# Kernel optimization log

Measured on AMD Instinct MI355X. Metric: run time of the kernel, lower is better.

The kernel has to match this reference:

```python
import jax, jax.numpy as jnp
import numpy as np

HID, STEM, BN_OUT, STEM_OUT, MLP = 256, 64, 128, 64, 128
BN_WS, STEM_WS = 5, 17
N, H_BN, W_BN, H_VIS, W_VIS = 4096, 128, 128, 1024, 1024


def setup_inputs() -> dict:
    key = jax.random.key(0)
    ks = jax.random.split(key, 24)
    f32 = jnp.float32
    def rn(k, shape, s=0.05):
        return jax.random.normal(k, shape, f32) * s
    return dict(
        bottleneck=rn(ks[0], (1, HID, H_BN, W_BN), 1.0),
        vis_stem_features=rn(ks[1], (1, STEM, H_VIS, W_VIS), 1.0),
        source_positions_vis=jax.random.uniform(ks[2], (N, 2), f32, 10.0, W_VIS - 10.0),
        pixel_to_sky=rn(ks[3], (N, 2, 2), 0.1),
        fused_h=H_BN, fused_w=W_BN, vis_h=H_VIS, vis_w=W_VIS,
        dw_w=rn(ks[4], (HID, 1, 7, 7)), dw_b=rn(ks[5], (HID,)),
        ln_g=jnp.ones((HID,), f32), ln_b=jnp.zeros((HID,), f32),
        pw1_w=rn(ks[6], (4 * HID, HID)), pw1_b=rn(ks[7], (4 * HID,)),
        pw2_w=rn(ks[8], (HID, 4 * HID)), pw2_b=rn(ks[9], (HID,)),
        cn_gamma=jnp.full((HID,), 1e-2, f32),
        bn1x1_w=rn(ks[10], (BN_OUT, HID, 1, 1)), bn1x1_b=rn(ks[11], (BN_OUT,)),
        st1_w=rn(ks[12], (STEM_OUT, STEM, 3, 3)), st1_b=rn(ks[13], (STEM_OUT,)),
        st2_w=rn(ks[14], (STEM_OUT, STEM_OUT, 3, 3)), st2_b=rn(ks[15], (STEM_OUT,)),
        h1_w=rn(ks[16], (MLP, BN_OUT + STEM_OUT)), h1_b=rn(ks[17], (MLP,)),
        h2_w=rn(ks[18], (MLP, MLP)), h2_b=rn(ks[19], (MLP,)),
        h3_w=rn(ks[20], (3, MLP)),
        h3_b=jnp.array([0.0, 0.0, float(np.log(0.05))], f32),
    )


def _gelu(x):
    return jax.nn.gelu(x, approximate=False)


def _conv2d(x, w, b, padding, groups=1):
    y = jax.lax.conv_general_dilated(
        x, w, (1, 1), [(padding, padding), (padding, padding)],
        dimension_numbers=('NCHW', 'OIHW', 'NCHW'), feature_group_count=groups)
    return y + b[None, :, None, None]


def _bilinear_windows(fm, pos, ws):
    """fm [1,C,H,W], pos [N,2] pixel coords -> [N,C,ws,ws].
    Matches torch grid_sample(mode=bilinear, padding=zeros, align_corners=True)
    with the module's normalize/unnormalize, i.e. direct pixel-coord sampling."""
    C, H, W = fm.shape[1:]
    fm2 = fm[0]
    half = ws // 2
    off = jnp.arange(-half, half + 1, dtype=pos.dtype)
    gy, gx = jnp.meshgrid(off, off, indexing='ij')
    xs = gx[None] + pos[:, 0, None, None]   # [N,ws,ws]
    ys = gy[None] + pos[:, 1, None, None]
    x0 = jnp.floor(xs); y0 = jnp.floor(ys)
    wx1 = xs - x0; wy1 = ys - y0
    x0i = x0.astype(jnp.int32); y0i = y0.astype(jnp.int32)
    def gather(yi, xi, w):
        valid = (yi >= 0) & (yi < H) & (xi >= 0) & (xi < W)
        v = fm2[:, jnp.clip(yi, 0, H - 1), jnp.clip(xi, 0, W - 1)]  # [C,N,ws,ws]
        return v * (w * valid)[None]
    out = (gather(y0i, x0i, (1 - wy1) * (1 - wx1))
           + gather(y0i, x0i + 1, (1 - wy1) * wx1)
           + gather(y0i + 1, x0i, wy1 * (1 - wx1))
           + gather(y0i + 1, x0i + 1, wy1 * wx1))
    return jnp.transpose(out, (1, 0, 2, 3))


def _gauss(ws):
    t = jnp.linspace(-1.0, 1.0, ws)
    yy, xx = jnp.meshgrid(t, t, indexing='ij')
    g = jnp.exp(-(xx ** 2 + yy ** 2) / (2 * 0.4 ** 2))
    return g / g.sum()


def _convnext(x, dw_w, dw_b, ln_g, ln_b, pw1_w, pw1_b, pw2_w, pw2_b, gamma):
    r = x
    x = _conv2d(x, dw_w, dw_b, padding=3, groups=x.shape[1])  # depthwise 7x7
    mu = x.mean(1, keepdims=True)
    var = ((x - mu) ** 2).mean(1, keepdims=True)
    x = (x - mu) / jnp.sqrt(var + 1e-6)
    x = x * ln_g[None, :, None, None] + ln_b[None, :, None, None]
    x = jnp.einsum('nchw,oc->nohw', x, pw1_w) + pw1_b[None, :, None, None]
    x = _gelu(x)
    x = jnp.einsum('nchw,oc->nohw', x, pw2_w) + pw2_b[None, :, None, None]
    return r + gamma[None, :, None, None] * x


def _forward(bottleneck, vis_stem_features, source_positions_vis, pixel_to_sky,
             dw_w, dw_b, ln_g, ln_b, pw1_w, pw1_b, pw2_w, pw2_b, cn_gamma,
             bn1x1_w, bn1x1_b, st1_w, st1_b, st2_w, st2_b,
             h1_w, h1_b, h2_w, h2_b, h3_w, h3_b,
             fused_h, fused_w, vis_h, vis_w):
    scale = jnp.array([fused_w / vis_w, fused_h / vis_h], source_positions_vis.dtype)
    pos_bn = source_positions_vis * scale
    # bottleneck branch: 5x5 windows -> ConvNeXt -> 1x1 conv -> GELU -> gauss pool
    bn_win = _bilinear_windows(bottleneck, pos_bn, BN_WS)              # [N,256,5,5]
    bn_feat = _convnext(bn_win, dw_w, dw_b, ln_g, ln_b, pw1_w, pw1_b, pw2_w, pw2_b, cn_gamma)
    bn_feat = _gelu(_conv2d(bn_feat, bn1x1_w, bn1x1_b, padding=0))     # [N,128,5,5]
    bn_vec = (bn_feat * _gauss(BN_WS)[None, None]).sum((-2, -1))       # [N,128]
    st_win = _bilinear_windows(vis_stem_features, source_positions_vis, STEM_WS)
    st = _gelu(_conv2d(st_win, st1_w, st1_b, padding=1))
    st = _gelu(_conv2d(st, st2_w, st2_b, padding=1))                   # [N,64,17,17]
    st_vec = (st * _gauss(STEM_WS)[None, None]).sum((-2, -1))          # [N,64]
    # head MLP
    x = jnp.concatenate([bn_vec, st_vec], axis=1)                      # [N,192]
    x = _gelu(x @ h1_w.T + h1_b)
    x = _gelu(x @ h2_w.T + h2_b)
    out = x @ h3_w.T + h3_b                                            # [N,3]
    dx_px, dy_px = out[:, 0], out[:, 1]
    log_sigma = jnp.clip(out[:, 2], -6.0, 3.0)
    pix = jnp.stack([dx_px, dy_px], axis=1)                            # [N,2]
    pred_sky = jnp.einsum('nij,nj->ni', pixel_to_sky, pix)             # [N,2]
    confidence = 1.0 / jnp.maximum(jnp.exp(log_sigma), 1e-4)
    return pred_sky, dx_px, dy_px, log_sigma, confidence


def reference(bottleneck, vis_stem_features, source_positions_vis, pixel_to_sky,
              fused_h, fused_w, vis_h, vis_w,
              dw_w, dw_b, ln_g, ln_b, pw1_w, pw1_b, pw2_w, pw2_b, cn_gamma,
              bn1x1_w, bn1x1_b, st1_w, st1_b, st2_w, st2_b,
              h1_w, h1_b, h2_w, h2_b, h3_w, h3_b):
    return _forward(bottleneck, vis_stem_features, source_positions_vis, pixel_to_sky,
                    dw_w, dw_b, ln_g, ln_b, pw1_w, pw1_b, pw2_w, pw2_b, cn_gamma,
                    bn1x1_w, bn1x1_b, st1_w, st1_b, st2_w, st2_b,
                    h1_w, h1_b, h2_w, h2_b, h3_w, h3_b,
                    fused_h, fused_w, vis_h, vis_w)
```

## Files before the change

kernel.cpp:

```cpp
#include <hip/hip_runtime.h>
#include <hip/hip_bf16.h>

#define XSTR 28

typedef short short8 __attribute__((ext_vector_type(8)));
typedef float f32x4  __attribute__((ext_vector_type(4)));
typedef float f32x16 __attribute__((ext_vector_type(16)));

__device__ __forceinline__ float gelu_f(float x){
    return 0.5f*x*(1.0f + erff(x*0.70710678118654752f));
}
__device__ __forceinline__ float gelu_q(float x){
    const float z = 1.5957691216057308f*x*(1.0f + 0.044715f*x*x);
    return x / (1.0f + __expf(-z));
}
__device__ __forceinline__ unsigned short f2bf(float f){
    unsigned int u = __float_as_uint(f);
    u += 0x7fffu + ((u>>16)&1u);
    return (unsigned short)(u>>16);
}
__device__ __forceinline__ unsigned int pack2(float a, float b){
    return (unsigned int)f2bf(a) | ((unsigned int)f2bf(b)<<16);
}
__device__ __forceinline__ float bf_lo(unsigned int u){ return __uint_as_float(u<<16); }
__device__ __forceinline__ float bf_hi(unsigned int u){ return __uint_as_float(u & 0xffff0000u); }
__device__ __forceinline__ float bfu(unsigned short v){ return __uint_as_float(((unsigned int)v)<<16); }

__device__ __forceinline__ void fma_row25(const float* __restrict__ row, float w, float* __restrict__ acc){
    const float4* r4 = (const float4*)row;
    float4 a0=r4[0], a1=r4[1], a2=r4[2], a3=r4[3], a4=r4[4], a5=r4[5];
    float a6 = row[24];
    acc[0]+=a0.x*w;  acc[1]+=a0.y*w;  acc[2]+=a0.z*w;  acc[3]+=a0.w*w;
    acc[4]+=a1.x*w;  acc[5]+=a1.y*w;  acc[6]+=a1.z*w;  acc[7]+=a1.w*w;
    acc[8]+=a2.x*w;  acc[9]+=a2.y*w;  acc[10]+=a2.z*w; acc[11]+=a2.w*w;
    acc[12]+=a3.x*w; acc[13]+=a3.y*w; acc[14]+=a3.z*w; acc[15]+=a3.w*w;
    acc[16]+=a4.x*w; acc[17]+=a4.y*w; acc[18]+=a4.z*w; acc[19]+=a4.w*w;
    acc[20]+=a5.x*w; acc[21]+=a5.y*w; acc[22]+=a5.z*w; acc[23]+=a5.w*w;
    acc[24]+=a6*w;
}

__global__ __launch_bounds__(512,4) void bn_branch_mfma(
    const float* __restrict__ bottleneck, const float* __restrict__ pos,
    const float* __restrict__ dw_w, const float* __restrict__ dw_b,
    const float* __restrict__ ln_g, const float* __restrict__ ln_b,
    const float* __restrict__ pw1_b, const float* __restrict__ pw2_b,
    const float* __restrict__ cn_gamma, const float* __restrict__ bn1x1_b,
    const short8* __restrict__ P1v, const short8* __restrict__ P2v,
    const short8* __restrict__ Pbv,
    float* __restrict__ vec_out)
{
    __shared__ __align__(16) unsigned char Xb[64*512];
    __shared__ __align__(16) unsigned char Hc[64*256];
    __shared__ float redA[400], redB[400], muS[56], rsS[56];

    const int n0 = blockIdx.x*2, t = threadIdx.x;
    const int lane = t & 63, w = t >> 6;
    const int mcol = lane & 15, h4 = lane >> 4;
    const int sP = t >> 8, cP = t & 255;

    unsigned int wvp[13];
    float xdw[25];
    {
        const int n = n0 + sP;
        const float px = pos[2*n]*0.125f, py = pos[2*n+1]*0.125f;
        const float fpx = floorf(px), fpy = floorf(py);
        const int ix0 = (int)fpx - 2, iy0 = (int)fpy - 2;
        const float fx = px - fpx, fy = py - fpy;
        const float w00=(1.f-fy)*(1.f-fx), w01=(1.f-fy)*fx, w10=fy*(1.f-fx), w11=fy*fx;
        float wv[25];
        {
            const float* fm = bottleneck + cP*16384;
            float P[6][6];
            #pragma unroll
            for (int r=0;r<6;r++){
                const int y = iy0+r;
                const bool yok = (y>=0)&&(y<128);
                const int yc = y<0?0:(y>127?127:y);
                #pragma unroll
                for (int s=0;s<6;s++){
                    const int x = ix0+s;
                    const bool ok = yok && (x>=0) && (x<128);
                    const int xc = x<0?0:(x>127?127:x);
                    P[r][s] = ok ? fm[yc*128+xc] : 0.f;
                }
            }
            #pragma unroll
            for (int a=0;a<5;a++)
            #pragma unroll
            for (int b=0;b<5;b++)
                wv[a*5+b] = w00*P[a][b]+w01*P[a][b+1]+w10*P[a+1][b]+w11*P[a+1][b+1];
        }
        #pragma unroll
        for (int i=0;i<12;i++) wvp[i] = pack2(wv[2*i], wv[2*i+1]);
        wvp[12] = pack2(wv[24], 0.f);
        {
            float wcr[49];
            const float* wc = dw_w + cP*49;
            #pragma unroll
            for (int k=0;k<49;k++) wcr[k]=wc[k];
            const float bb = dw_b[cP];
            #pragma unroll
            for (int i=0;i<5;i++){
                #pragma unroll
                for (int j=0;j<5;j++){
                    float a = bb;
                    #pragma unroll
                    for (int u=0;u<7;u++){
                        const int y = i+u-3;
                        if (y<0||y>4) continue;
                        #pragma unroll
                        for (int v=0;v<7;v++){
                            const int x = j+v-3;
                            if (x<0||x>4) continue;
                            a += wv[y*5+x]*wcr[u*7+v];
                        }
                    }
                    xdw[i*5+j] = a;
                }
            }
        }
        #pragma unroll
        for (int p=0;p<25;p++){
            const int row = sP*32 + p;
            *(unsigned short*)(Xb + row*512 + ((2*cP) ^ ((row&7)<<4))) = f2bf(xdw[p]);
        }
    }
    __syncthreads();
    if (t < 400){
        const int sp = t>>3, part = t&7;
        const int row = (sp/25)*32 + (sp - (sp/25)*25);
        float a=0.f, b=0.f;
        for (int c=part; c<256; c+=8){
            const float v = bfu(*(const unsigned short*)(Xb + row*512 + ((2*c) ^ ((row&7)<<4))));
            a += v; b += v*v;
        }
        redA[t]=a; redB[t]=b;
    }
    __syncthreads();
    if (t < 50){
        float a=0.f, b=0.f;
        #pragma unroll
        for (int s=0;s<8;s++){ a+=redA[t*8+s]; b+=redB[t*8+s]; }
        const float m = a*(1.f/256.f);
        const float var = b*(1.f/256.f) - m*m;
        muS[t]=m; rsS[t]=rsqrtf(var+1e-6f);
    }
    __syncthreads();
    {
        const float g = ln_g[cP], bb = ln_b[cP];
        #pragma unroll
        for (int p=0;p<25;p++){
            const int row = sP*32 + p;
            const float v = (xdw[p]-muS[sP*25+p])*rsS[sP*25+p]*g + bb;
            *(unsigned short*)(Xb + row*512 + ((2*cP) ^ ((row&7)<<4))) = f2bf(v);
        }
    }
    __syncthreads();

    f32x4 acc2[2][4];
    #pragma unroll
    for (int ml=0;ml<2;ml++)
        #pragma unroll
        for (int nt=0;nt<4;nt++) acc2[ml][nt]=0.f;

    for (int ch=0; ch<8; ++ch){
        const int mt = ch*8 + w;
        f32x4 a1[4];
        #pragma unroll
        for (int nt=0;nt<4;nt++) a1[nt]=0.f;
        #pragma unroll
        for (int kk=0; kk<8; ++kk){
            const short8 av = P1v[((mt<<3)+kk)*64 + lane];
            #pragma unroll
            for (int nt=0; nt<4; ++nt){
                const int row = nt*16 + mcol;
                const int ad = row*512 + ((kk*64 + h4*16) ^ ((row&7)<<4));
                const short8 bv = *(const short8*)(Xb + ad);
                a1[nt] = __builtin_amdgcn_mfma_f32_16x16x32_bf16(av, bv, a1[nt], 0,0,0);
            }
        }
        {
            const float4 b1v = *(const float4*)(pw1_b + mt*16 + h4*4);
            #pragma unroll
            for (int nt=0; nt<4; ++nt){
                const int row = nt*16 + mcol;
                const float g0 = gelu_q(a1[nt].x + b1v.x);
                const float g1 = gelu_q(a1[nt].y + b1v.y);
                const float g2 = gelu_q(a1[nt].z + b1v.z);
                const float g3 = gelu_q(a1[nt].w + b1v.w);
                const int ad = row*256 + ((w*32 + h4*8) ^ ((row&7)<<4));
                *(uint2*)(Hc + ad) = make_uint2(pack2(g0,g1), pack2(g2,g3));
            }
        }
        __syncthreads();
        #pragma unroll
        for (int ml=0; ml<2; ++ml){
            const int mtc = w*2 + ml;
            #pragma unroll
            for (int kk2=0; kk2<4; ++kk2){
                const short8 av = P2v[(mtc*32 + (ch*4 + kk2))*64 + lane];
                #pragma unroll
                for (int nt=0; nt<4; ++nt){
                    const int row = nt*16 + mcol;
                    const int ad = row*256 + ((kk2*64 + h4*16) ^ ((row&7)<<4));
                    const short8 bv = *(const short8*)(Hc + ad);
                    acc2[ml][nt] = __builtin_amdgcn_mfma_f32_16x16x32_bf16(av, bv, acc2[ml][nt], 0,0,0);
                }
            }
        }
        __syncthreads();
    }

    #pragma unroll
    for (int ml=0; ml<2; ++ml){
        const int c0 = (w*2+ml)*16 + h4*4;
        const float4 gm = *(const float4*)(cn_gamma + c0);
        const float4 b2 = *(const float4*)(pw2_b + c0);
        #pragma unroll
        for (int nt=0; nt<4; ++nt){
            const int row = nt*16 + mcol;
            const int ad = row*512 + ((2*c0) ^ ((row&7)<<4));
            const float f0 = gm.x*(acc2[ml][nt].x + b2.x);
            const float f1 = gm.y*(acc2[ml][nt].y + b2.y);
            const float f2 = gm.z*(acc2[ml][nt].z + b2.z);
            const float f3 = gm.w*(acc2[ml][nt].w + b2.w);
            *(uint2*)(Xb + ad) = make_uint2(pack2(f0,f1), pack2(f2,f3));
        }
    }
    __syncthreads();
    #pragma unroll
    for (int p=0;p<25;p++){
        const int row = sP*32 + p;
        unsigned short* ptr = (unsigned short*)(Xb + row*512 + ((2*cP) ^ ((row&7)<<4)));
        const float r = (p&1) ? bf_hi(wvp[p>>1]) : bf_lo(wvp[p>>1]);
        *ptr = f2bf(bfu(*ptr) + r);
    }
    __syncthreads();

    {
        f32x4 a3[4];
        #pragma unroll
        for (int nt=0;nt<4;nt++) a3[nt]=0.f;
        #pragma unroll
        for (int kk=0; kk<8; ++kk){
            const short8 av = Pbv[((w<<3)+kk)*64 + lane];
            #pragma unroll
            for (int nt=0; nt<4; ++nt){
                const int row = nt*16 + mcol;
                const int ad = row*512 + ((kk*64 + h4*16) ^ ((row&7)<<4));
                const short8 bv = *(const short8*)(Xb + ad);
                a3[nt] = __builtin_amdgcn_mfma_f32_16x16x32_bf16(av, bv, a3[nt], 0,0,0);
            }
        }
        const float4 bb = *(const float4*)(bn1x1_b + w*16 + h4*4);
        float e5[5];
        #pragma unroll
        for (int a=0;a<5;a++){
            const float ta = -1.f + 0.5f*a;
            e5[a] = expf(-3.125f*ta*ta);
        }
        const float Sv = e5[0]+e5[1]+e5[2]+e5[3]+e5[4];
        const float invS = 1.0f/(Sv*Sv);
        float sA[2][4];
        #pragma unroll
        for (int s=0;s<2;s++)
            #pragma unroll
            for (int j=0;j<4;j++) sA[s][j]=0.f;
        #pragma unroll
        for (int nt=0; nt<4; ++nt){
            const int row = nt*16 + mcol;
            const int s = row>>5, p = row&31;
            if (p < 25){
                const int pa = p/5, pb = p - pa*5;
                const float g = e5[pa]*e5[pb];
                sA[s][0] += g*gelu_q(a3[nt].x + bb.x);
                sA[s][1] += g*gelu_q(a3[nt].y + bb.y);
                sA[s][2] += g*gelu_q(a3[nt].z + bb.z);
                sA[s][3] += g*gelu_q(a3[nt].w + bb.w);
            }
        }
        #pragma unroll
        for (int off=1; off<16; off<<=1){
            #pragma unroll
            for (int s=0;s<2;s++)
                #pragma unroll
                for (int j=0;j<4;j++) sA[s][j] += __shfl_xor(sA[s][j], off);
        }
        if (mcol == 0){
            const int o = w*16 + h4*4;
            #pragma unroll
            for (int s=0;s<2;s++){
                float* vo = vec_out + (n0+s)*192 + o;
                vo[0]=sA[s][0]*invS; vo[1]=sA[s][1]*invS;
                vo[2]=sA[s][2]*invS; vo[3]=sA[s][3]*invS;
            }
        }
    }
}

__global__ __launch_bounds__(256) void prepack_bn_kernel(
    const float* __restrict__ W1, const float* __restrict__ W2, const float* __restrict__ Wb,
    unsigned short* __restrict__ P1, unsigned short* __restrict__ P2, unsigned short* __restrict__ Pb)
{
    const int tid = blockIdx.x*256 + threadIdx.x;
    const float* src; unsigned short* dst; int row, col, stride, idx;
    if (tid < 32768){
        idx = tid;
        const int frag = idx>>6, l = idx&63;
        row = (frag>>3)*16 + (l&15); col = (frag&7)*32 + (l>>4)*8; stride = 256;
        src = W1; dst = P1;
    } else if (tid < 65536){
        idx = tid - 32768;
        const int frag = idx>>6, l = idx&63;
        row = (frag>>5)*16 + (l&15); col = (frag&31)*32 + (l>>4)*8; stride = 1024;
        src = W2; dst = P2;
    } else if (tid < 69632){
        idx = tid - 65536;
        const int frag = idx>>6, l = idx&63;
        row = (frag>>3)*16 + (l&15); col = (frag&7)*32 + (l>>4)*8; stride = 256;
        src = Wb; dst = Pb;
    } else return;
    const float* s = src + row*stride + col;
    unsigned int v[4];
    #pragma unroll
    for (int j=0;j<4;j++) v[j] = pack2(s[2*j], s[2*j+1]);
    *(uint4*)(dst + (size_t)idx*8) = make_uint4(v[0],v[1],v[2],v[3]);
}

__global__ __launch_bounds__(256,2) void bn_branch_valu(
    const float* __restrict__ bottleneck, const float* __restrict__ pos,
    const float* __restrict__ dw_w, const float* __restrict__ dw_b,
    const float* __restrict__ ln_g, const float* __restrict__ ln_b,
    const float* __restrict__ pw1_w, const float* __restrict__ pw1_b,
    const float* __restrict__ pw2_w, const float* __restrict__ pw2_b,
    const float* __restrict__ cn_gamma,
    const float* __restrict__ bn1x1_w, const float* __restrict__ bn1x1_b,
    float* __restrict__ vec_out)
{
    __shared__ float xln[256*XSTR];
    __shared__ float hbuf[256*XSTR];
    __shared__ float redA[200], redB[200];
    __shared__ float mu[25], rs[25];

    const int n = blockIdx.x;
    const int t = threadIdx.x;
    const int c = t;

    const float px = pos[2*n]*0.125f, py = pos[2*n+1]*0.125f;
    const float fpx = floorf(px), fpy = floorf(py);
    const int ix0 = (int)fpx - 2, iy0 = (int)fpy - 2;
    const float fx = px - fpx, fy = py - fpy;
    const float w00=(1.f-fy)*(1.f-fx), w01=(1.f-fy)*fx, w10=fy*(1.f-fx), w11=fy*fx;

    float wv[25];
    {
        const float* fm = bottleneck + c*16384;
        float P[6][6];
        #pragma unroll
        for (int r=0;r<6;r++){
            const int y = iy0+r;
            const bool yok = (y>=0)&&(y<128);
            const int yc = y<0?0:(y>127?127:y);
            #pragma unroll
            for (int s=0;s<6;s++){
                const int x = ix0+s;
                const bool ok = yok && (x>=0) && (x<128);
                const int xc = x<0?0:(x>127?127:x);
                P[r][s] = ok ? fm[yc*128+xc] : 0.f;
            }
        }
        #pragma unroll
        for (int a=0;a<5;a++)
        #pragma unroll
        for (int b=0;b<5;b++)
            wv[a*5+b] = w00*P[a][b]+w01*P[a][b+1]+w10*P[a+1][b]+w11*P[a+1][b+1];
    }
    {
        float wcr[49];
        const float* wc = dw_w + c*49;
        #pragma unroll
        for (int k=0;k<49;k++) wcr[k]=wc[k];
        const float bb = dw_b[c];
        #pragma unroll
        for (int i=0;i<5;i++){
            #pragma unroll
            for (int j=0;j<5;j++){
                float a = bb;
                #pragma unroll
                for (int u=0;u<7;u++){
                    const int y = i+u-3;
                    if (y<0||y>4) continue;
                    #pragma unroll
                    for (int v=0;v<7;v++){
                        const int x = j+v-3;
                        if (x<0||x>4) continue;
                        a += wv[y*5+x]*wcr[u*7+v];
                    }
                }
                xln[c*XSTR + i*5+j] = a;
            }
        }
    }
    __syncthreads();
    if (t < 200){
        const int p = t>>3, s = t&7;
        float a=0.f, b=0.f;
        for (int cc=s; cc<256; cc+=8){
            const float v = xln[cc*XSTR+p];
            a += v; b += v*v;
        }
        redA[t]=a; redB[t]=b;
    }
    __syncthreads();
    if (t < 25){
        float a=0.f, b=0.f;
        #pragma unroll
        for (int s=0;s<8;s++){ a+=redA[t*8+s]; b+=redB[t*8+s]; }
        const float m = a*(1.f/256.f);
        const float var = b*(1.f/256.f) - m*m;
        mu[t]=m; rs[t]=rsqrtf(var+1e-6f);
    }
    __syncthreads();
    {
        const float g = ln_g[c], bb = ln_b[c];
        #pragma unroll
        for (int p=0;p<25;p++)
            xln[c*XSTR+p] = (xln[c*XSTR+p]-mu[p])*rs[p]*g + bb;
    }
    __syncthreads();
    float acc2[25];
    #pragma unroll
    for (int p=0;p<25;p++) acc2[p]=0.f;
    for (int r=0;r<4;r++){
        const int o = r*256 + t;
        float h[25];
        {
            const float b1 = pw1_b[o];
            #pragma unroll
            for (int p=0;p<25;p++) h[p]=b1;
            const float* wr = pw1_w + o*256;
            for (int cc=0;cc<256;cc++)
                fma_row25(xln + cc*XSTR, wr[cc], h);
            #pragma unroll
            for (int p=0;p<25;p++) h[p]=gelu_f(h[p]);
        }
        __syncthreads();
        #pragma unroll
        for (int p=0;p<25;p++) hbuf[t*XSTR+p]=h[p];
        __syncthreads();
        {
            const float* w2 = pw2_w + t*1024 + r*256;
            for (int k=0;k<256;k++)
                fma_row25(hbuf + k*XSTR, w2[k], acc2);
        }
    }
    {
        const float gam = cn_gamma[c], b2 = pw2_b[c];
        #pragma unroll
        for (int p=0;p<25;p++)
            xln[c*XSTR+p] = wv[p] + gam*(acc2[p]+b2);
    }
    __syncthreads();
    if (t < 128){
        float acc[25];
        #pragma unroll
        for (int p=0;p<25;p++) acc[p]=0.f;
        const float* wr = bn1x1_w + t*256;
        for (int cc=0;cc<256;cc++)
            fma_row25(xln + cc*XSTR, wr[cc], acc);
        const float b = bn1x1_b[t];
        float e5[5];
        #pragma unroll
        for (int a=0;a<5;a++){
            const float ta = -1.f + 0.5f*a;
            e5[a] = expf(-3.125f*ta*ta);
        }
        const float Sv = e5[0]+e5[1]+e5[2]+e5[3]+e5[4];
        float res = 0.f;
        #pragma unroll
        for (int a=0;a<5;a++){
            float rowa = 0.f;
            #pragma unroll
            for (int bb=0;bb<5;bb++)
                rowa += e5[bb]*gelu_f(acc[a*5+bb]+b);
            res += e5[a]*rowa;
        }
        vec_out[n*192+t] = res/(Sv*Sv);
    }
}

__global__ __launch_bounds__(256) void prepack_kernel(
    const float* __restrict__ W1, const float* __restrict__ W2,
    unsigned short* __restrict__ Ap)
{
    const int tid = blockIdx.x*256 + threadIdx.x;
    if (tid >= 9216) return;
    const int conv = tid / 4608;
    const int r = tid - conv*4608;
    const int frag = r >> 6, l = r & 63;
    const int k  = frag >> 3;
    const int kt = (frag >> 1) & 3;
    const int wo = frag & 1;
    const float* W = conv ? W2 : W1;
    const int o  = wo*32 + (l & 31);
    const int c0 = kt*16 + (l >> 5)*8;
    unsigned int v[4];
    #pragma unroll
    for (int jj=0; jj<4; jj++){
        const float f0 = W[o*576 + (c0+2*jj  )*9 + k];
        const float f1 = W[o*576 + (c0+2*jj+1)*9 + k];
        v[jj] = pack2(f0, f1);
    }
    *(uint4*)(Ap + (size_t)tid*8) = make_uint4(v[0], v[1], v[2], v[3]);
}

#define STEM_CONV32(SRC, AP)                                                        \
    for (int k=0;k<9;k++){                                                          \
        const unsigned short* trow = sTab + m*90 + nh*45 + k;                       \
        int tj[5];                                                                  \
        _Pragma("unroll")                                                           \
        for (int j=0;j<5;j++) tj[j] = trow[j*9];                                    \
        _Pragma("unroll")                                                           \
        for (int kt=0;kt<4;kt++){                                                   \
            const short8 av = (AP)[(k*8 + kt*2 + wo)*64 + lane];                    \
            const int cb = kt*32 + hi16;                                            \
            _Pragma("unroll")                                                       \
            for (int j=0;j<5;j++){                                                  \
                const short8 bv = *(const short8*)((SRC) + (tj[j] ^ cb));           \
                acc[j] = __builtin_amdgcn_mfma_f32_32x32x16_bf16(av, bv, acc[j], 0,0,0); \
            }                                                                       \
        }                                                                           \
    }

__global__ __launch_bounds__(256,2) void stem_branch_kernel(
    const float* __restrict__ vis,
    const float* __restrict__ pos,
    const short8* __restrict__ Ap1,
    const float* __restrict__ st1_b,
    const float* __restrict__ st2_b,
    float* __restrict__ vec_out)
{
    __shared__ __align__(16) unsigned char sXt[290*128];
    __shared__ __align__(16) unsigned char sC1[290*128];
    __shared__ unsigned short sTab[32*90];
    __shared__ float redS[64][2];

    const int n = blockIdx.x;
    const int t = threadIdx.x;
    const int lane = t & 63;
    const int m = lane & 31;
    const int hi = lane >> 5;
    const int hi16 = hi*16;
    const int w = t >> 6;
    const int wo = w & 1;
    const int nh = w >> 1;

    const float fpx0 = pos[2*n], fpy0 = pos[2*n+1];
    const float fpx = floorf(fpx0), fpy = floorf(fpy0);
    const int ix0 = (int)fpx - 8, iy0 = (int)fpy - 8;
    const float fx = fpx0-fpx, fy = fpy0-fpy;
    const float w00=(1.f-fy)*(1.f-fx), w01=(1.f-fy)*fx, w10=fy*(1.f-fx), w11=fy*fx;

    if (t < 32)      *(unsigned int*)(sXt + 289*128 + t*4) = 0u;
    else if (t < 64) *(unsigned int*)(sC1 + 289*128 + (t-32)*4) = 0u;

    for (int idx = t; idx < 32*90; idx += 256){
        const int mm = idx/90, rem = idx - mm*90;
        const int nt = rem/9, k = rem - nt*9;
        const int p = nt*32 + mm;
        int pp = 289;
        if (p < 289){
            const int py = (p*241)>>12, px = p - py*17;
            const int y = py + k/3 - 1, x = px + (k - (k/3)*3) - 1;
            if (((unsigned)y < 17u) && ((unsigned)x < 17u)) pp = y*17 + x;
        }
        sTab[idx] = (unsigned short)(pp*128 + ((pp&7)<<4));
    }

    for (int task = t; task < 64*17; task += 256){
        const int c  = task & 63;
        const int py = task >> 6;
        const float* r0 = vis + c*1048576 + (iy0+py)*1024 + ix0;
        float a[18], b[18];
        #pragma unroll
        for (int kk=0; kk<18; kk++){ a[kk]=r0[kk]; b[kk]=r0[1024+kk]; }
        #pragma unroll
        for (int px=0; px<17; px++){
            const float v = w00*a[px] + w01*a[px+1] + w10*b[px] + w11*b[px+1];
            const int p = py*17 + px;
            *(unsigned short*)(sXt + p*128 + ((2*c) ^ ((p&7)<<4))) = f2bf(v);
        }
    }
    __syncthreads();

    f32x16 acc[5];
    #pragma unroll
    for (int j=0;j<5;j++) acc[j] = 0.f;
    STEM_CONV32(sXt, Ap1)

    {
        float4 b4[4];
        #pragma unroll
        for (int rg=0;rg<4;rg++) b4[rg] = *(const float4*)(st1_b + wo*32 + 8*rg + 4*hi);
        #pragma unroll
        for (int j=0;j<5;j++){
            const int p = (nh*5+j)*32 + m;
            if (p < 289){
                const int swz = (p&7)<<4;
                #pragma unroll
                for (int rg=0;rg<4;rg++){
                    const int ch0 = wo*32 + 8*rg + 4*hi;
                    const float v0 = gelu_q(acc[j][4*rg+0] + b4[rg].x);
                    const float v1 = gelu_q(acc[j][4*rg+1] + b4[rg].y);
                    const float v2 = gelu_q(acc[j][4*rg+2] + b4[rg].z);
                    const float v3 = gelu_q(acc[j][4*rg+3] + b4[rg].w);
                    *(uint2*)(sC1 + p*128 + ((2*ch0) ^ swz)) = make_uint2(pack2(v0,v1), pack2(v2,v3));
                }
            }
        }
    }
    __syncthreads();

    const short8* Ap2 = Ap1 + 4608;
    #pragma unroll
    for (int j=0;j<5;j++) acc[j] = 0.f;
    STEM_CONV32(sC1, Ap2)

    {
        float4 b4[4];
        #pragma unroll
        for (int rg=0;rg<4;rg++) b4[rg] = *(const float4*)(st2_b + wo*32 + 8*rg + 4*hi);
        float s[16];
        #pragma unroll
        for (int r=0;r<16;r++) s[r]=0.f;
        #pragma unroll
        for (int j=0;j<5;j++){
            const int p = (nh*5+j)*32 + m;
            if (p < 289){
                const int py = (p*241)>>12;
                const int px = p - py*17;
                const float ty = -1.f + 0.125f*py;
                const float tx = -1.f + 0.125f*px;
                const float g = expf(-3.125f*(ty*ty + tx*tx));
                #pragma unroll
                for (int rg=0;rg<4;rg++){
                    s[4*rg+0] += g*gelu_q(acc[j][4*rg+0] + b4[rg].x);
                    s[4*rg+1] += g*gelu_q(acc[j][4*rg+1] + b4[rg].y);
                    s[4*rg+2] += g*gelu_q(acc[j][4*rg+2] + b4[rg].z);
                    s[4*rg+3] += g*gelu_q(acc[j][4*rg+3] + b4[rg].w);
                }
            }
        }
        #pragma unroll
        for (int off=1; off<32; off<<=1){
            #pragma unroll
            for (int r=0;r<16;r++) s[r] += __shfl_xor(s[r], off);
        }
        if (m == 0){
            #pragma unroll
            for (int rg=0;rg<4;rg++)
                #pragma unroll
                for (int e=0;e<4;e++)
                    redS[wo*32 + 8*rg + 4*hi + e][nh] = s[4*rg+e];
        }
    }
    __syncthreads();
    if (t < 64){
        float Sv = 0.f;
        #pragma unroll
        for (int j=0;j<17;j++){
            const float tj = -1.f + 0.125f*j;
            Sv += expf(-3.125f*tj*tj);
        }
        vec_out[n*192+128+t] = (redS[t][0] + redS[t][1]) / (Sv*Sv);
    }
}

__global__ __launch_bounds__(128) void head16_kernel(
    const float* __restrict__ vec, const float* __restrict__ p2s,
    const float* __restrict__ h1_w, const float* __restrict__ h1_b,
    const float* __restrict__ h2_w, const float* __restrict__ h2_b,
    const float* __restrict__ h3_w, const float* __restrict__ h3_b,
    float* __restrict__ out, int N)
{
    __shared__ float v[16][192];
    __shared__ float x1s[16][132];
    __shared__ float x2s[16][132];
    __shared__ float o3s[16][4];
    const int n0 = blockIdx.x*16, t = threadIdx.x;

    for (int idx=t; idx<16*192; idx+=128){
        const int s = idx/192, k = idx - s*192;
        v[s][k] = vec[n0*192 + idx];
    }
    __syncthreads();
    {
        const int o = t;
        float acc[16];
        const float b = h1_b[o];
        #pragma unroll
        for (int s=0;s<16;s++) acc[s]=b;
        const float4* wr = (const float4*)(h1_w + o*192);
        for (int k4=0;k4<48;k4++){
            const float4 wv4 = wr[k4];
            #pragma unroll
            for (int s=0;s<16;s++){
                const float4 vv = *(const float4*)&v[s][k4*4];
                acc[s] += wv4.x*vv.x + wv4.y*vv.y + wv4.z*vv.z + wv4.w*vv.w;
            }
        }
        #pragma unroll
        for (int s=0;s<16;s++) x1s[s][o] = gelu_f(acc[s]);
    }
    __syncthreads();
    {
        const int o = t;
        float acc[16];
        const float b = h2_b[o];
        #pragma unroll
        for (int s=0;s<16;s++) acc[s]=b;
        const float4* wr = (const float4*)(h2_w + o*128);
        for (int k4=0;k4<32;k4++){
            const float4 wv4 = wr[k4];
            #pragma unroll
            for (int s=0;s<16;s++){
                const float4 vv = *(const float4*)&x1s[s][k4*4];
                acc[s] += wv4.x*vv.x + wv4.y*vv.y + wv4.z*vv.z + wv4.w*vv.w;
            }
        }
        #pragma unroll
        for (int s=0;s<16;s++) x2s[s][o] = gelu_f(acc[s]);
    }
    __syncthreads();
    if (t < 48){
        const int j = t>>4, s = t&15;
        float a = h3_b[j];
        const float* wr = h3_w + j*128;
        for (int k=0;k<128;k++) a += x2s[s][k]*wr[k];
        o3s[s][j] = a;
    }
    __syncthreads();
    if (t < 16){
        const int s = t, n = n0 + s;
        const float dx = o3s[s][0], dy = o3s[s][1];
        float ls = o3s[s][2];
        ls = ls < -6.f ? -6.f : (ls > 3.f ? 3.f : ls);
        const float s0 = p2s[n*4+0]*dx + p2s[n*4+1]*dy;
        const float s1 = p2s[n*4+2]*dx + p2s[n*4+3]*dy;
        const float conf = 1.0f/fmaxf(expf(ls), 1e-4f);
        out[2*n]   = s0;
        out[2*n+1] = s1;
        out[2*N+n] = dx;
        out[3*N+n] = dy;
        out[4*N+n] = ls;
        out[5*N+n] = conf;
    }
}

extern "C" void kernel_launch(void* const* d_in, const int* in_sizes, int n_in,
                              void* d_out, int out_size, void* d_ws, size_t ws_size,
                              hipStream_t stream)
{
    (void)n_in; (void)out_size;
    const float* bottleneck = (const float*)d_in[0];
    const float* vis        = (const float*)d_in[1];
    const float* pos        = (const float*)d_in[2];
    const float* p2s        = (const float*)d_in[3];
    const float* dw_w  = (const float*)d_in[8];
    const float* dw_b  = (const float*)d_in[9];
    const float* ln_g  = (const float*)d_in[10];
    const float* ln_b  = (const float*)d_in[11];
    const float* pw1_w = (const float*)d_in[12];
    const float* pw1_b = (const float*)d_in[13];
    const float* pw2_w = (const float*)d_in[14];
    const float* pw2_b = (const float*)d_in[15];
    const float* gam   = (const float*)d_in[16];
    const float* b1w   = (const float*)d_in[17];
    const float* b1b   = (const float*)d_in[18];
    const float* s1w   = (const float*)d_in[19];
    const float* s1b   = (const float*)d_in[20];
    const float* s2w   = (const float*)d_in[21];
    const float* s2b   = (const float*)d_in[22];
    const float* h1w   = (const float*)d_in[23];
    const float* h1b   = (const float*)d_in[24];
    const float* h2w   = (const float*)d_in[25];
    const float* h2b   = (const float*)d_in[26];
    const float* h3w   = (const float*)d_in[27];
    const float* h3b   = (const float*)d_in[28];

    const int N = in_sizes[2]/2;
    float* vec = (float*)d_ws;
    const size_t vec_bytes = (size_t)N*192*sizeof(float);
    unsigned short* Apack = (unsigned short*)((char*)d_ws + vec_bytes);
    unsigned short* P1 = Apack + 73728;
    unsigned short* P2 = P1 + 262144;
    unsigned short* Pb = P2 + 262144;
    const size_t need = vec_bytes + 147456u + (262144u+262144u+32768u)*2u;

    hipMemsetAsync(d_ws, 0, vec_bytes, stream);

    prepack_kernel<<<36, 256, 0, stream>>>(s1w, s2w, Apack);

    if (ws_size >= need){
        prepack_bn_kernel<<<272, 256, 0, stream>>>(pw1_w, pw2_w, b1w, P1, P2, Pb);
        bn_branch_mfma<<<N/2, 512, 0, stream>>>(bottleneck, pos, dw_w, dw_b, ln_g, ln_b,
                                                pw1_b, pw2_b, gam, b1b,
                                                (const short8*)P1, (const short8*)P2, (const short8*)Pb,
                                                vec);
    } else {
        bn_branch_valu<<<N, 256, 0, stream>>>(bottleneck, pos, dw_w, dw_b, ln_g, ln_b,
                                              pw1_w, pw1_b, pw2_w, pw2_b, gam, b1w, b1b, vec);
    }
    stem_branch_kernel<<<N, 256, 0, stream>>>(vis, pos, (const short8*)Apack, s1b, s2b, vec);
    head16_kernel<<<N/16, 128, 0, stream>>>(vec, p2s, h1w, h1b, h2w, h2b, h3w, h3b,
                                            (float*)d_out, N);
}
```

Measured before the change: 824.8 us.

## Split stem conv across 8 waves and reuse one shared buffer for both layers

The stem branch block grows from 256 to 512 threads. Each wave pair now owns up to 3 of the 10 spatial 32-pixel tiles instead of 5, which cuts accumulator registers and raises launch bounds to (512,4). The conv1 output is kept in registers, and after a barrier it is written back over the input shared buffer, so the separate sC1 buffer is removed and LDS per block roughly halves. The cost is an extra barrier, uneven tile counts across waves, and more redundant A-fragment loads per block.

```diff
diff --git a/kernel.cpp b/kernel.cpp
--- a/kernel.cpp
+++ b/kernel.cpp
@@ -516,23 +516,25 @@
 
 #define STEM_CONV32(SRC, AP)                                                        \
     for (int k=0;k<9;k++){                                                          \
-        const unsigned short* trow = sTab + m*90 + nh*45 + k;                       \
-        int tj[5];                                                                  \
+        int tj[3];                                                                  \
         _Pragma("unroll")                                                           \
-        for (int j=0;j<5;j++) tj[j] = trow[j*9];                                    \
+        for (int j=0;j<3;j++)                                                       \
+            tj[j] = (int)sTab[m*90 + (j<cnt ? st+j : st)*9 + k];                    \
         _Pragma("unroll")                                                           \
         for (int kt=0;kt<4;kt++){                                                   \
             const short8 av = (AP)[(k*8 + kt*2 + wo)*64 + lane];                    \
             const int cb = kt*32 + hi16;                                            \
             _Pragma("unroll")                                                       \
-            for (int j=0;j<5;j++){                                                  \
-                const short8 bv = *(const short8*)((SRC) + (tj[j] ^ cb));           \
-                acc[j] = __builtin_amdgcn_mfma_f32_32x32x16_bf16(av, bv, acc[j], 0,0,0); \
+            for (int j=0;j<3;j++){                                                  \
+                if (j < cnt){                                                       \
+                    const short8 bv = *(const short8*)((SRC) + (tj[j] ^ cb));       \
+                    acc[j] = __builtin_amdgcn_mfma_f32_32x32x16_bf16(av, bv, acc[j], 0,0,0); \
+                }                                                                   \
             }                                                                       \
         }                                                                           \
     }
 
-__global__ __launch_bounds__(256,2) void stem_branch_kernel(
+__global__ __launch_bounds__(512,4) void stem_branch_kernel(
     const float* __restrict__ vis,
     const float* __restrict__ pos,
     const short8* __restrict__ Ap1,
@@ -541,9 +543,8 @@
     float* __restrict__ vec_out)
 {
     __shared__ __align__(16) unsigned char sXt[290*128];
-    __shared__ __align__(16) unsigned char sC1[290*128];
     __shared__ unsigned short sTab[32*90];
-    __shared__ float redS[64][2];
+    __shared__ float redS[64][4];
 
     const int n = blockIdx.x;
     const int t = threadIdx.x;
@@ -554,6 +555,8 @@
     const int w = t >> 6;
     const int wo = w & 1;
     const int nh = w >> 1;
+    const int st  = nh*3 - (nh==3 ? 1 : 0);
+    const int cnt = (nh < 2) ? 3 : 2;
 
     const float fpx0 = pos[2*n], fpy0 = pos[2*n+1];
     const float fpx = floorf(fpx0), fpy = floorf(fpy0);
@@ -561,10 +564,9 @@
     const float fx = fpx0-fpx, fy = fpy0-fpy;
     const float w00=(1.f-fy)*(1.f-fx), w01=(1.f-fy)*fx, w10=fy*(1.f-fx), w11=fy*fx;
 
-    if (t < 32)      *(unsigned int*)(sXt + 289*128 + t*4) = 0u;
-    else if (t < 64) *(unsigned int*)(sC1 + 289*128 + (t-32)*4) = 0u;
-
-    for (int idx = t; idx < 32*90; idx += 256){
+    if (t < 32) *(unsigned int*)(sXt + 289*128 + t*4) = 0u;
+
+    for (int idx = t; idx < 32*90; idx += 512){
         const int mm = idx/90, rem = idx - mm*90;
         const int nt = rem/9, k = rem - nt*9;
         const int p = nt*32 + mm;
@@ -577,7 +579,7 @@
         sTab[idx] = (unsigned short)(pp*128 + ((pp&7)<<4));
     }
 
-    for (int task = t; task < 64*17; task += 256){
+    for (int task = t; task < 64*17; task += 512){
         const int c  = task & 63;
         const int py = task >> 6;
         const float* r0 = vis + c*1048576 + (iy0+py)*1024 + ix0;
@@ -593,28 +595,42 @@
     }
     __syncthreads();
 
-    f32x16 acc[5];
+    f32x16 acc[3];
     #pragma unroll
-    for (int j=0;j<5;j++) acc[j] = 0.f;
+    for (int j=0;j<3;j++) acc[j] = 0.f;
     STEM_CONV32(sXt, Ap1)
 
+    uint2 pk[3][4];
     {
         float4 b4[4];
         #pragma unroll
         for (int rg=0;rg<4;rg++) b4[rg] = *(const float4*)(st1_b + wo*32 + 8*rg + 4*hi);
         #pragma unroll
-        for (int j=0;j<5;j++){
-            const int p = (nh*5+j)*32 + m;
+        for (int j=0;j<3;j++){
+            if (j < cnt){
+                #pragma unroll
+                for (int rg=0;rg<4;rg++){
+                    const float v0 = gelu_q(acc[j][4*rg+0] + b4[rg].x);
+                    const float v1 = gelu_q(acc[j][4*rg+1] + b4[rg].y);
+                    const float v2 = gelu_q(acc[j][4*rg+2] + b4[rg].z);
+                    const float v3 = gelu_q(acc[j][4*rg+3] + b4[rg].w);
+                    pk[j][rg] = make_uint2(pack2(v0,v1), pack2(v2,v3));
+                }
+            }
+        }
+    }
+    __syncthreads();
+
+    #pragma unroll
+    for (int j=0;j<3;j++){
+        if (j < cnt){
+            const int p = (st+j)*32 + m;
             if (p < 289){
                 const int swz = (p&7)<<4;
                 #pragma unroll
                 for (int rg=0;rg<4;rg++){
                     const int ch0 = wo*32 + 8*rg + 4*hi;
-                    const float v0 = gelu_q(acc[j][4*rg+0] + b4[rg].x);
-                    const float v1 = gelu_q(acc[j][4*rg+1] + b4[rg].y);
-                    const float v2 = gelu_q(acc[j][4*rg+2] + b4[rg].z);
-                    const float v3 = gelu_q(acc[j][4*rg+3] + b4[rg].w);
-                    *(uint2*)(sC1 + p*128 + ((2*ch0) ^ swz)) = make_uint2(pack2(v0,v1), pack2(v2,v3));
+                    *(uint2*)(sXt + p*128 + ((2*ch0) ^ swz)) = pk[j][rg];
                 }
             }
         }
@@ -623,8 +639,8 @@
 
     const short8* Ap2 = Ap1 + 4608;
     #pragma unroll
-    for (int j=0;j<5;j++) acc[j] = 0.f;
-    STEM_CONV32(sC1, Ap2)
+    for (int j=0;j<3;j++) acc[j] = 0.f;
+    STEM_CONV32(sXt, Ap2)
 
     {
         float4 b4[4];
@@ -634,20 +650,22 @@
         #pragma unroll
         for (int r=0;r<16;r++) s[r]=0.f;
         #pragma unroll
-        for (int j=0;j<5;j++){
-            const int p = (nh*5+j)*32 + m;
-            if (p < 289){
-                const int py = (p*241)>>12;
-                const int px = p - py*17;
-                const float ty = -1.f + 0.125f*py;
-                const float tx = -1.f + 0.125f*px;
-                const float g = expf(-3.125f*(ty*ty + tx*tx));
-                #pragma unroll
-                for (int rg=0;rg<4;rg++){
-                    s[4*rg+0] += g*gelu_q(acc[j][4*rg+0] + b4[rg].x);
-                    s[4*rg+1] += g*gelu_q(acc[j][4*rg+1] + b4[rg].y);
-                    s[4*rg+2] += g*gelu_q(acc[j][4*rg+2] + b4[rg].z);
-                    s[4*rg+3] += g*gelu_q(acc[j][4*rg+3] + b4[rg].w);
+        for (int j=0;j<3;j++){
+            if (j < cnt){
+                const int p = (st+j)*32 + m;
+                if (p < 289){
+                    const int py = (p*241)>>12;
+                    const int px = p - py*17;
+                    const float ty = -1.f + 0.125f*py;
+                    const float tx = -1.f + 0.125f*px;
+                    const float g = expf(-3.125f*(ty*ty + tx*tx));
+                    #pragma unroll
+                    for (int rg=0;rg<4;rg++){
+                        s[4*rg+0] += g*gelu_q(acc[j][4*rg+0] + b4[rg].x);
+                        s[4*rg+1] += g*gelu_q(acc[j][4*rg+1] + b4[rg].y);
+                        s[4*rg+2] += g*gelu_q(acc[j][4*rg+2] + b4[rg].z);
+                        s[4*rg+3] += g*gelu_q(acc[j][4*rg+3] + b4[rg].w);
+                    }
                 }
             }
         }
@@ -672,7 +690,7 @@
             const float tj = -1.f + 0.125f*j;
             Sv += expf(-3.125f*tj*tj);
         }
-        vec_out[n*192+128+t] = (redS[t][0] + redS[t][1]) / (Sv*Sv);
+        vec_out[n*192+128+t] = (redS[t][0] + redS[t][1] + redS[t][2] + redS[t][3]) / (Sv*Sv);
     }
 }
 
@@ -811,7 +829,7 @@
         bn_branch_valu<<<N, 256, 0, stream>>>(bottleneck, pos, dw_w, dw_b, ln_g, ln_b,
                                               pw1_w, pw1_b, pw2_w, pw2_b, gam, b1w, b1b, vec);
     }
-    stem_branch_kernel<<<N, 256, 0, stream>>>(vis, pos, (const short8*)Apack, s1b, s2b, vec);
+    stem_branch_kernel<<<N, 512, 0, stream>>>(vis, pos, (const short8*)Apack, s1b, s2b, vec);
     head16_kernel<<<N/16, 128, 0, stream>>>(vec, p2s, h1w, h1b, h2w, h2b, h3w, h3b,
                                             (float*)d_out, N);
 }
```

Result: no change. 840.5 us (+1.9%).
